# Optimization experiments

Measured on AMD Instinct MI355X. Metric: run time of the kernel, lower is better.

The kernel has to match this reference:

```python
import jax, jax.numpy as jnp
import numpy as np

B, D, H1, H2 = 512, 1024, 512, 128

def setup_inputs() -> dict:
    key = jax.random.key(0)
    ks = jax.random.split(key, 3)
    x = jax.random.normal(ks[0], (B, D), dtype=jnp.float32)
    W1 = jax.random.normal(ks[1], (H1, D), dtype=jnp.float32)
    W2 = jax.random.normal(ks[2], (H2, H1), dtype=jnp.float32)
    b1 = jnp.full((H1,), 0.1, dtype=jnp.float32)
    b2 = jnp.full((H2,), 0.1, dtype=jnp.float32)
    b3 = jnp.full((H1,), 0.1, dtype=jnp.float32)
    b_r = jnp.full((D,), 0.1, dtype=jnp.float32)
    return {"x": x, "W1": W1, "b1": b1, "W2": W2, "b2": b2, "b3": b3, "b_r": b_r}

def reference(x, W1, b1, W2, b2, b3, b_r):
    # encoder
    c1 = jax.nn.sigmoid(x @ W1.T + b1)          # [B, H1]
    c2 = jax.nn.sigmoid(c1 @ W2.T + b2)         # [B, H2]
    # decoder (tied weights)
    c3 = jax.nn.sigmoid(c2 @ W2 + b3)           # [B, H1]
    recover = c3 @ W1 + b_r                     # [B, D]
    # Jacobian of code w.r.t. x, batched (replaces per-sample diag+matmul loop):
    # Jac[b] = diag(c2'(b)) @ W2 @ diag(c1'(b)) @ W1
    s1p = c1 * (1.0 - c1)                       # [B, H1]
    s2p = c2 * (1.0 - c2)                       # [B, H2]
    M = s2p[:, :, None] * W2[None, :, :] * s1p[:, None, :]   # [B, H2, H1]
    Jac = jnp.einsum('bhk,kd->bhd', M, W1)      # [B, H2, D]
    return (recover, c2, Jac)
```

## Files before the change

kernel.cpp:

```cpp
#include <hip/hip_runtime.h>


typedef _Float16 f16x8 __attribute__((ext_vector_type(8)));
typedef _Float16 f16x4 __attribute__((ext_vector_type(4)));
typedef float    f32x4 __attribute__((ext_vector_type(4)));
typedef float    f32x2 __attribute__((ext_vector_type(2)));

__device__ __forceinline__ void gld_lds16(const _Float16* src, _Float16* dst_wave_uniform) {
    __builtin_amdgcn_global_load_lds((const __attribute__((address_space(1))) unsigned int*)src,
                                     (__attribute__((address_space(3))) unsigned int*)dst_wave_uniform,
                                     16, 0, 0);
}

__device__ __forceinline__ void prep_dev(int bx, const float* __restrict__ W1,
                                         const float* __restrict__ W2,
                                         _Float16* __restrict__ W1T,
                                         _Float16* __restrict__ W2h) {
    if (bx < 512) {
        __shared__ float tile[32][33];
        int dt = (bx & 31) * 32, kt = (bx >> 5) * 32;
        int tx = threadIdx.x & 31, ty = threadIdx.x >> 5;
        #pragma unroll
        for (int r = 0; r < 32; r += 8)
            tile[ty + r][tx] = W1[(kt + ty + r) * 1024 + dt + tx];
        __syncthreads();
        #pragma unroll
        for (int r = 0; r < 32; r += 8)
            W1T[(size_t)(dt + ty + r) * 512 + kt + tx] = (_Float16)tile[tx][ty + r];
    } else {
        int i = (bx - 512) * 1024 + threadIdx.x * 4;
        f32x4 v = *(const f32x4*)(W2 + i);
        f16x4 h;
        h.x = (_Float16)v.x; h.y = (_Float16)v.y; h.z = (_Float16)v.z; h.w = (_Float16)v.w;
        *(f16x4*)(W2h + i) = h;
    }
}

template <int EPI, bool TRANSB>
__device__ void gemm_dev(const float* __restrict__ A, const float* __restrict__ Bm,
                         const float* __restrict__ bias,
                         float* __restrict__ C, float* __restrict__ Cd,
                         _Float16* __restrict__ Ch,
                         int M, int N, int K, int m0, int n0) {
    __shared__ __align__(16) float As[32][34];
    __shared__ __align__(16) float Bs[32][68];
    const int tid = threadIdx.x, tx = tid & 15, ty = tid >> 4;
    const int ka  = tid & 31, ma  = tid >> 5;
    const int kbt = tid & 31, nbt = tid >> 5;
    const int nbf = tid & 63, kbf = tid >> 6;
    float acc[2][4] = {};
    float rA[4], rB[8];

    #pragma unroll
    for (int r = 0; r < 4; ++r) rA[r] = A[(size_t)(m0 + ma + 8 * r) * K + ka];
    if (TRANSB) {
        #pragma unroll
        for (int r = 0; r < 8; ++r) rB[r] = Bm[(size_t)(n0 + nbt + 8 * r) * K + kbt];
    } else {
        #pragma unroll
        for (int r = 0; r < 8; ++r) rB[r] = Bm[(size_t)(kbf + 4 * r) * N + n0 + nbf];
    }

    for (int k0 = 0; k0 < K; k0 += 32) {
        #pragma unroll
        for (int r = 0; r < 4; ++r) As[ka][ma + 8 * r] = rA[r];
        if (TRANSB) {
            #pragma unroll
            for (int r = 0; r < 8; ++r) Bs[kbt][nbt + 8 * r] = rB[r];
        } else {
            #pragma unroll
            for (int r = 0; r < 8; ++r) Bs[kbf + 4 * r][nbf] = rB[r];
        }
        const int k1 = k0 + 32;
        if (k1 < K) {
            #pragma unroll
            for (int r = 0; r < 4; ++r) rA[r] = A[(size_t)(m0 + ma + 8 * r) * K + k1 + ka];
            if (TRANSB) {
                #pragma unroll
                for (int r = 0; r < 8; ++r) rB[r] = Bm[(size_t)(n0 + nbt + 8 * r) * K + k1 + kbt];
            } else {
                #pragma unroll
                for (int r = 0; r < 8; ++r) rB[r] = Bm[(size_t)(k1 + kbf + 4 * r) * N + n0 + nbf];
            }
        }
        __syncthreads();
        #pragma unroll
        for (int k = 0; k < 32; ++k) {
            f32x2 av = *(const f32x2*)&As[k][ty * 2];
            f32x4 bv = *(const f32x4*)&Bs[k][tx * 4];
            #pragma unroll
            for (int i = 0; i < 2; ++i)
                #pragma unroll
                for (int j = 0; j < 4; ++j)
                    acc[i][j] += av[i] * bv[j];
        }
        __syncthreads();
    }

    #pragma unroll
    for (int i = 0; i < 2; ++i) {
        int row = m0 + ty * 2 + i;
        #pragma unroll
        for (int j = 0; j < 4; ++j) {
            int col = n0 + tx * 4 + j;
            float z = acc[i][j] + bias[col];
            float s = 1.f / (1.f + __expf(-z));
            if constexpr (EPI == 1) {
                C[(size_t)row * N + col]  = s;
                Cd[(size_t)row * N + col] = s * (1.f - s);
            } else {
                Ch[(size_t)row * N + col] = (_Float16)s;
            }
        }
    }
}

__global__ __launch_bounds__(256) void fused_prep_gemm1(const float* __restrict__ x,
                                                        const float* __restrict__ W1,
                                                        const float* __restrict__ b1,
                                                        const float* __restrict__ W2,
                                                        _Float16* __restrict__ W1T,
                                                        _Float16* __restrict__ W2h,
                                                        float* __restrict__ c1,
                                                        float* __restrict__ s1p) {
    int bx = blockIdx.x;
    if (bx < 128) {
        gemm_dev<1, true>(x, W1, b1, c1, s1p, nullptr, 512, 512, 1024,
                          (bx >> 3) * 32, (bx & 7) * 64);
    } else {
        prep_dev(bx - 128, W1, W2, W1T, W2h);
    }
}

__global__ __launch_bounds__(256) void gemm2_kernel(const float* __restrict__ c1,
                                                    const float* __restrict__ W2,
                                                    const float* __restrict__ b2,
                                                    float* __restrict__ out_c2,
                                                    float* __restrict__ s2p) {
    gemm_dev<1, true>(c1, W2, b2, out_c2, s2p, nullptr, 512, 128, 512,
                      blockIdx.y * 32, blockIdx.x * 64);
}

__global__ __launch_bounds__(256) void gemm3_kernel(const float* __restrict__ out_c2,
                                                    const float* __restrict__ W2,
                                                    const float* __restrict__ b3,
                                                    _Float16* __restrict__ c3h) {
    gemm_dev<2, false>(out_c2, W2, b3, nullptr, nullptr, c3h, 512, 512, 128,
                       (blockIdx.x >> 3) * 32, (blockIdx.x & 7) * 64);
}

__global__ __launch_bounds__(256, 4) void jacW_fused(const _Float16* __restrict__ c3h,
                                                     const _Float16* __restrict__ W2h,
                                                     const _Float16* __restrict__ W1T,
                                                     const float* __restrict__ s1p,
                                                     const float* __restrict__ s2p,
                                                     const float* __restrict__ br,
                                                     float* __restrict__ out_rec,
                                                     float* __restrict__ out_jac) {
    __shared__ __align__(16) _Float16 Wsl[128 * 64];
    __shared__ __align__(16) _Float16 Bsl[128 * 64];
    __shared__ _Float16 S1h[512];
    __shared__ float    S2s[128];

    const int tid = threadIdx.x;
    const int lane = tid & 63, wave = tid >> 6;
    const int wm = (wave >> 1) * 64, wn = (wave & 1) * 64;
    const int l15 = lane & 15, q = lane >> 4;
    const int bid = blockIdx.x;

    const bool is_rec = (bid < 32);
    const _Float16* Abase;
    float* outp;
    int n0, b = 0, m0 = 0;
    if (is_rec) {
        m0 = (bid >> 3) * 128; n0 = (bid & 7) * 128;
        Abase = c3h + (size_t)m0 * 512;
        outp = out_rec + (size_t)m0 * 1024;
        if (tid < 128) S2s[tid] = br[n0 + tid];
    } else {
        int jid = bid - 32;
        int w = (jid & 7) * 512 + (jid >> 3);
        b = w >> 3; n0 = (w & 7) * 128;
        Abase = W2h;
        outp = out_jac + (size_t)b * (128 * 1024);
        S1h[tid]       = (_Float16)s1p[(size_t)b * 512 + tid];
        S1h[tid + 256] = (_Float16)s1p[(size_t)b * 512 + 256 + tid];
        if (tid < 128) S2s[tid] = s2p[(size_t)b * 128 + tid];
    }

    const int srow = wave * 8 + (lane >> 3);
    const int skof = ((lane & 7) ^ (lane >> 3)) * 8;
    const _Float16* Bbase = W1T + (size_t)n0 * 512;

    f32x4 acc[4][4];
    #pragma unroll
    for (int i = 0; i < 4; ++i)
        #pragma unroll
        for (int j = 0; j < 4; ++j) acc[i][j] = (f32x4){0.f, 0.f, 0.f, 0.f};

    for (int t = 0; t < 8; ++t) {
        const int kb = t * 64;
        #pragma unroll
        for (int r = 0; r < 4; ++r) {
            gld_lds16(Abase + (size_t)(r * 32 + srow) * 512 + kb + skof, Wsl + (r * 32 + wave * 8) * 64);
            gld_lds16(Bbase + (size_t)(r * 32 + srow) * 512 + kb + skof, Bsl + (r * 32 + wave * 8) * 64);
        }
        __syncthreads();
        #pragma unroll
        for (int kk = 0; kk < 64; kk += 32) {
            f16x8 af[4], bf[4], sf;
            if (!is_rec)
                sf = *(const f16x8*)(&S1h[kb + kk + q * 8]);
            #pragma unroll
            for (int i = 0; i < 4; ++i) {
                f16x8 wf = *(const f16x8*)(Wsl + (wm + i * 16 + l15) * 64 + ((kk + q * 8) ^ ((l15 & 7) * 8)));
                af[i] = is_rec ? wf : wf * sf;
            }
            #pragma unroll
            for (int j = 0; j < 4; ++j)
                bf[j] = *(const f16x8*)(Bsl + (wn + j * 16 + l15) * 64 + ((kk + q * 8) ^ ((l15 & 7) * 8)));
            #pragma unroll
            for (int i = 0; i < 4; ++i)
                #pragma unroll
                for (int j = 0; j < 4; ++j)
                    acc[i][j] = __builtin_amdgcn_mfma_f32_16x16x32_f16(af[i], bf[j], acc[i][j], 0, 0, 0);
        }
        __syncthreads();
    }

    #pragma unroll
    for (int i = 0; i < 4; ++i) {
        #pragma unroll
        for (int rg = 0; rg < 4; ++rg) {
            int ml = wm + i * 16 + q * 4 + rg;
            float rs = is_rec ? 1.f : S2s[ml];
            #pragma unroll
            for (int j = 0; j < 4; ++j) {
                int cl = wn + j * 16 + l15;
                float v = acc[i][j][rg] * rs;
                if (is_rec) v += S2s[cl];
                __builtin_nontemporal_store(v, outp + (size_t)ml * 1024 + n0 + cl);
            }
        }
    }
}

extern "C" void kernel_launch(void* const* d_in, const int* in_sizes, int n_in,
                              void* d_out, int out_size, void* d_ws, size_t ws_size,
                              hipStream_t stream) {
    const float* x  = (const float*)d_in[0];
    const float* W1 = (const float*)d_in[1];
    const float* b1 = (const float*)d_in[2];
    const float* W2 = (const float*)d_in[3];
    const float* b2 = (const float*)d_in[4];
    const float* b3 = (const float*)d_in[5];
    const float* br = (const float*)d_in[6];

    float* out_rec = (float*)d_out;
    float* out_c2  = out_rec + 512 * 1024;
    float* out_jac = out_c2 + 512 * 128;

    char* ws = (char*)d_ws;
    _Float16* W1T = (_Float16*)(ws);
    _Float16* W2h = (_Float16*)(ws + 0x100000);
    float*    c1  = (float*)(ws + 0x120000);
    float*    s1p = (float*)(ws + 0x220000);
    float*    s2p = (float*)(ws + 0x320000);
    _Float16* c3h = (_Float16*)(ws + 0x360000);

    fused_prep_gemm1<<<704, 256, 0, stream>>>(x, W1, b1, W2, W1T, W2h, c1, s1p);
    gemm2_kernel<<<dim3(2, 16), 256, 0, stream>>>(c1, W2, b2, out_c2, s2p);
    gemm3_kernel<<<128, 256, 0, stream>>>(out_c2, W2, b3, c3h);
    jacW_fused<<<4128, 256, 0, stream>>>(c3h, W2h, W1T, s1p, s2p, br, out_rec, out_jac);
}
```

Measured before the change: 405.5 us.

## Process two batch samples per Jacobian block to reuse staged weight tiles

Each Jacobian block now computes two consecutive batch samples against the same W2/W1T tiles staged in LDS, halving global-to-LDS tile loads and B-fragment LDS reads per output. The reconstruction path is split into its own early-return branch, which removes per-iteration is_rec selects. The grid shrinks accordingly and launch bounds drop to 2 blocks per CU, since accumulator registers double. Lower occupancy may reduce the latency hiding available for the large output stores.

After: 404.3 us. Within noise of the previous version (-0.3%).

```diff
diff --git a/kernel.cpp b/kernel.cpp
--- a/kernel.cpp
+++ b/kernel.cpp
@@ -149,7 +149,7 @@
                        (blockIdx.x >> 3) * 32, (blockIdx.x & 7) * 64);
 }
 
-__global__ __launch_bounds__(256, 4) void jacW_fused(const _Float16* __restrict__ c3h,
+__global__ __launch_bounds__(256, 2) void jacW_fused(const _Float16* __restrict__ c3h,
                                                      const _Float16* __restrict__ W2h,
                                                      const _Float16* __restrict__ W1T,
                                                      const float* __restrict__ s1p,
@@ -159,8 +159,8 @@
                                                      float* __restrict__ out_jac) {
     __shared__ __align__(16) _Float16 Wsl[128 * 64];
     __shared__ __align__(16) _Float16 Bsl[128 * 64];
-    __shared__ _Float16 S1h[512];
-    __shared__ float    S2s[128];
+    __shared__ _Float16 S1h[2][512];
+    __shared__ float    S2s[2][128];
 
     const int tid = threadIdx.x;
     const int lane = tid & 63, wave = tid >> 6;
@@ -168,78 +168,132 @@
     const int l15 = lane & 15, q = lane >> 4;
     const int bid = blockIdx.x;
 
-    const bool is_rec = (bid < 32);
-    const _Float16* Abase;
-    float* outp;
-    int n0, b = 0, m0 = 0;
-    if (is_rec) {
-        m0 = (bid >> 3) * 128; n0 = (bid & 7) * 128;
-        Abase = c3h + (size_t)m0 * 512;
-        outp = out_rec + (size_t)m0 * 1024;
-        if (tid < 128) S2s[tid] = br[n0 + tid];
-    } else {
-        int jid = bid - 32;
-        int w = (jid & 7) * 512 + (jid >> 3);
-        b = w >> 3; n0 = (w & 7) * 128;
-        Abase = W2h;
-        outp = out_jac + (size_t)b * (128 * 1024);
-        S1h[tid]       = (_Float16)s1p[(size_t)b * 512 + tid];
-        S1h[tid + 256] = (_Float16)s1p[(size_t)b * 512 + 256 + tid];
-        if (tid < 128) S2s[tid] = s2p[(size_t)b * 128 + tid];
-    }
-
     const int srow = wave * 8 + (lane >> 3);
     const int skof = ((lane & 7) ^ (lane >> 3)) * 8;
+
+    if (bid < 32) {
+        const int m0 = (bid >> 3) * 128, n0 = (bid & 7) * 128;
+        const _Float16* Abase = c3h + (size_t)m0 * 512;
+        const _Float16* Bbase = W1T + (size_t)n0 * 512;
+        float* outp = out_rec + (size_t)m0 * 1024;
+        if (tid < 128) S2s[0][tid] = br[n0 + tid];
+
+        f32x4 acc[4][4];
+        #pragma unroll
+        for (int i = 0; i < 4; ++i)
+            #pragma unroll
+            for (int j = 0; j < 4; ++j) acc[i][j] = (f32x4){0.f, 0.f, 0.f, 0.f};
+
+        for (int t = 0; t < 8; ++t) {
+            const int kb = t * 64;
+            #pragma unroll
+            for (int r = 0; r < 4; ++r) {
+                gld_lds16(Abase + (size_t)(r * 32 + srow) * 512 + kb + skof, Wsl + (r * 32 + wave * 8) * 64);
+                gld_lds16(Bbase + (size_t)(r * 32 + srow) * 512 + kb + skof, Bsl + (r * 32 + wave * 8) * 64);
+            }
+            __syncthreads();
+            #pragma unroll
+            for (int kk = 0; kk < 64; kk += 32) {
+                f16x8 af[4], bf[4];
+                #pragma unroll
+                for (int i = 0; i < 4; ++i)
+                    af[i] = *(const f16x8*)(Wsl + (wm + i * 16 + l15) * 64 + ((kk + q * 8) ^ ((l15 & 7) * 8)));
+                #pragma unroll
+                for (int j = 0; j < 4; ++j)
+                    bf[j] = *(const f16x8*)(Bsl + (wn + j * 16 + l15) * 64 + ((kk + q * 8) ^ ((l15 & 7) * 8)));
+                #pragma unroll
+                for (int i = 0; i < 4; ++i)
+                    #pragma unroll
+                    for (int j = 0; j < 4; ++j)
+                        acc[i][j] = __builtin_amdgcn_mfma_f32_16x16x32_f16(af[i], bf[j], acc[i][j], 0, 0, 0);
+            }
+            __syncthreads();
+        }
+
+        #pragma unroll
+        for (int i = 0; i < 4; ++i) {
+            #pragma unroll
+            for (int rg = 0; rg < 4; ++rg) {
+                int ml = wm + i * 16 + q * 4 + rg;
+                #pragma unroll
+                for (int j = 0; j < 4; ++j) {
+                    int cl = wn + j * 16 + l15;
+                    __builtin_nontemporal_store(acc[i][j][rg] + S2s[0][cl],
+                                                outp + (size_t)ml * 1024 + n0 + cl);
+                }
+            }
+        }
+        return;
+    }
+
+    const int jid = bid - 32;
+    const int w = (jid & 7) * 256 + (jid >> 3);
+    const int pair = w >> 3, n0 = (w & 7) * 128;
+    const int bA = pair * 2;
+
+    S1h[0][tid]       = (_Float16)s1p[(size_t)bA * 512 + tid];
+    S1h[0][tid + 256] = (_Float16)s1p[(size_t)bA * 512 + 256 + tid];
+    S1h[1][tid]       = (_Float16)s1p[(size_t)(bA + 1) * 512 + tid];
+    S1h[1][tid + 256] = (_Float16)s1p[(size_t)(bA + 1) * 512 + 256 + tid];
+    if (tid < 128) S2s[0][tid] = s2p[(size_t)bA * 128 + tid];
+    else           S2s[1][tid - 128] = s2p[(size_t)(bA + 1) * 128 + (tid - 128)];
+
     const _Float16* Bbase = W1T + (size_t)n0 * 512;
 
-    f32x4 acc[4][4];
+    f32x4 accA[4][4], accB[4][4];
     #pragma unroll
     for (int i = 0; i < 4; ++i)
         #pragma unroll
-        for (int j = 0; j < 4; ++j) acc[i][j] = (f32x4){0.f, 0.f, 0.f, 0.f};
+        for (int j = 0; j < 4; ++j) {
+            accA[i][j] = (f32x4){0.f, 0.f, 0.f, 0.f};
+            accB[i][j] = (f32x4){0.f, 0.f, 0.f, 0.f};
+        }
 
     for (int t = 0; t < 8; ++t) {
         const int kb = t * 64;
         #pragma unroll
         for (int r = 0; r < 4; ++r) {
-            gld_lds16(Abase + (size_t)(r * 32 + srow) * 512 + kb + skof, Wsl + (r * 32 + wave * 8) * 64);
+            gld_lds16(W2h   + (size_t)(r * 32 + srow) * 512 + kb + skof, Wsl + (r * 32 + wave * 8) * 64);
             gld_lds16(Bbase + (size_t)(r * 32 + srow) * 512 + kb + skof, Bsl + (r * 32 + wave * 8) * 64);
         }
         __syncthreads();
         #pragma unroll
         for (int kk = 0; kk < 64; kk += 32) {
-            f16x8 af[4], bf[4], sf;
-            if (!is_rec)
-                sf = *(const f16x8*)(&S1h[kb + kk + q * 8]);
-            #pragma unroll
-            for (int i = 0; i < 4; ++i) {
-                f16x8 wf = *(const f16x8*)(Wsl + (wm + i * 16 + l15) * 64 + ((kk + q * 8) ^ ((l15 & 7) * 8)));
-                af[i] = is_rec ? wf : wf * sf;
-            }
+            const f16x8 sfA = *(const f16x8*)(&S1h[0][kb + kk + q * 8]);
+            const f16x8 sfB = *(const f16x8*)(&S1h[1][kb + kk + q * 8]);
+            f16x8 bf[4];
             #pragma unroll
             for (int j = 0; j < 4; ++j)
                 bf[j] = *(const f16x8*)(Bsl + (wn + j * 16 + l15) * 64 + ((kk + q * 8) ^ ((l15 & 7) * 8)));
             #pragma unroll
-            for (int i = 0; i < 4; ++i)
+            for (int i = 0; i < 4; ++i) {
+                const f16x8 wf = *(const f16x8*)(Wsl + (wm + i * 16 + l15) * 64 + ((kk + q * 8) ^ ((l15 & 7) * 8)));
+                f16x8 af = wf * sfA;
                 #pragma unroll
                 for (int j = 0; j < 4; ++j)
-                    acc[i][j] = __builtin_amdgcn_mfma_f32_16x16x32_f16(af[i], bf[j], acc[i][j], 0, 0, 0);
-        }
-        __syncthreads();
-    }
-
+                    accA[i][j] = __builtin_amdgcn_mfma_f32_16x16x32_f16(af, bf[j], accA[i][j], 0, 0, 0);
+                af = wf * sfB;
+                #pragma unroll
+                for (int j = 0; j < 4; ++j)
+                    accB[i][j] = __builtin_amdgcn_mfma_f32_16x16x32_f16(af, bf[j], accB[i][j], 0, 0, 0);
+            }
+        }
+        __syncthreads();
+    }
+
+    float* outA = out_jac + (size_t)bA * (128 * 1024);
+    float* outB = outA + (128 * 1024);
     #pragma unroll
     for (int i = 0; i < 4; ++i) {
         #pragma unroll
         for (int rg = 0; rg < 4; ++rg) {
             int ml = wm + i * 16 + q * 4 + rg;
-            float rs = is_rec ? 1.f : S2s[ml];
+            float rsA = S2s[0][ml], rsB = S2s[1][ml];
             #pragma unroll
             for (int j = 0; j < 4; ++j) {
                 int cl = wn + j * 16 + l15;
-                float v = acc[i][j][rg] * rs;
-                if (is_rec) v += S2s[cl];
-                __builtin_nontemporal_store(v, outp + (size_t)ml * 1024 + n0 + cl);
+                __builtin_nontemporal_store(accA[i][j][rg] * rsA, outA + (size_t)ml * 1024 + n0 + cl);
+                __builtin_nontemporal_store(accB[i][j][rg] * rsB, outB + (size_t)ml * 1024 + n0 + cl);
             }
         }
     }
@@ -271,5 +325,5 @@
     fused_prep_gemm1<<<704, 256, 0, stream>>>(x, W1, b1, W2, W1T, W2h, c1, s1p);
     gemm2_kernel<<<dim3(2, 16), 256, 0, stream>>>(c1, W2, b2, out_c2, s2p);
     gemm3_kernel<<<128, 256, 0, stream>>>(out_c2, W2, b3, c3h);
-    jacW_fused<<<4128, 256, 0, stream>>>(c3h, W2h, W1T, s1p, s2p, br, out_rec, out_jac);
-}
+    jacW_fused<<<2080, 256, 0, stream>>>(c3h, W2h, W1T, s1p, s2p, br, out_rec, out_jac);
+}
```
